# Kernel optimization log

Measured on AMD Instinct MI355X. Metric: run time of the kernel, lower is better.

The kernel has to match this reference:

```python
import jax, jax.numpy as jnp
import numpy as np

N_NODES = 50000
N_EDGES = 800000
D_FEAT = 128
EMBED_DIM = 128
NUM_HEADS = 8
HEAD_DIM = EMBED_DIM // NUM_HEADS


def mish(x):
    return x * jnp.tanh(jax.nn.softplus(x))


def setup_inputs() -> dict:
    key = jax.random.key(0)
    ks = jax.random.split(key, 8)
    nodes = jax.random.normal(ks[0], (N_NODES, D_FEAT), dtype=jnp.float32)
    senders = jax.random.randint(ks[1], (N_EDGES,), 0, N_NODES, dtype=jnp.int32)
    receivers = jax.random.randint(ks[2], (N_EDGES,), 0, N_NODES, dtype=jnp.int32)
    s = 1.0 / np.sqrt(D_FEAT)
    Ws_k = jax.random.normal(ks[3], (D_FEAT, NUM_HEADS, HEAD_DIM), dtype=jnp.float32) * s
    Ws_b = jnp.zeros((NUM_HEADS, HEAD_DIM), dtype=jnp.float32)
    Wr_k = jax.random.normal(ks[4], (D_FEAT, NUM_HEADS, HEAD_DIM), dtype=jnp.float32) * s
    Wr_b = jnp.zeros((NUM_HEADS, HEAD_DIM), dtype=jnp.float32)
    attn_k = jax.random.normal(ks[5], (HEAD_DIM, 1), dtype=jnp.float32) / np.sqrt(HEAD_DIM)
    attn_b = jnp.zeros((1,), dtype=jnp.float32)
    return {"nodes": nodes, "senders": senders, "receivers": receivers,
            "Ws_k": Ws_k, "Ws_b": Ws_b, "Wr_k": Wr_k, "Wr_b": Wr_b,
            "attn_k": attn_k, "attn_b": attn_b}


def reference(nodes, senders, receivers, Ws_k, Ws_b, Wr_k, Wr_b, attn_k, attn_b):
    # gather endpoint features along edges
    sent = nodes[senders]        # [E, F]
    recv = nodes[receivers]      # [E, F]
    # edge messages: W_s(sent) -> [E, H, D]
    edges = jnp.einsum('ef,fhd->ehd', sent, Ws_k) + Ws_b
    # attention logits: Dense(1)(mish(edges + W_r(recv))) -> [E, H, 1]
    x = mish(edges + jnp.einsum('ef,fhd->ehd', recv, Wr_k) + Wr_b)
    logits = jnp.einsum('ehd,do->eho', x, attn_k) + attn_b  # [E, H, 1]
    # segment softmax over incoming edges of each receiver node
    seg_max = jax.ops.segment_max(logits, receivers, num_segments=N_NODES)  # [N, H, 1]
    unnorm = jnp.exp(logits - seg_max[receivers])
    denom = jax.ops.segment_sum(unnorm, receivers, num_segments=N_NODES)   # [N, H, 1]
    weights = unnorm / denom[receivers]                                     # [E, H, 1]
    # attention-weighted scatter-add into receiver nodes
    agg = jax.ops.segment_sum(edges * weights, receivers, num_segments=N_NODES)  # [N, H, D]
    # node update: concat heads
    return agg.reshape(N_NODES, NUM_HEADS * HEAD_DIM)
```

## Files before the change

### kernel.cpp

```cpp
#include <hip/hip_runtime.h>

#define N_NODES 50000
#define N_EDGES 800000
#define HEADS 8
#define HD 16
#define F 128
#define RPB 16
#define SCAN_B 1024
#define NB1 ((N_NODES + SCAN_B - 1) / SCAN_B)
#define TILE 8

__device__ __forceinline__ float head16_sum(float x) {
    int v;
    v = __builtin_amdgcn_update_dpp(0, __float_as_int(x), 0xB1, 0xF, 0xF, true);
    x += __int_as_float(v);
    v = __builtin_amdgcn_update_dpp(0, __float_as_int(x), 0x4E, 0xF, 0xF, true);
    x += __int_as_float(v);
    v = __builtin_amdgcn_update_dpp(0, __float_as_int(x), 0x141, 0xF, 0xF, true);
    x += __int_as_float(v);
    v = __builtin_amdgcn_update_dpp(0, __float_as_int(x), 0x140, 0xF, 0xF, true);
    x += __int_as_float(v);
    return x;
}

__global__ __launch_bounds__(128) void k_proj(
        const float* __restrict__ nodes,
        const float* __restrict__ Ws, const float* __restrict__ Wsb,
        const float* __restrict__ Wr, const float* __restrict__ Wrb,
        float* __restrict__ Ps, float* __restrict__ Pr) {
    __shared__ float rows[RPB][F];
    const int o  = threadIdx.x;
    const int r0 = blockIdx.x * RPB;
    for (int i = 0; i < RPB; ++i)
        rows[i][o] = nodes[(r0 + i) * F + o];
    __syncthreads();

    float accs[RPB], accr[RPB];
    const float bs = Wsb[o], br = Wrb[o];
    #pragma unroll
    for (int i = 0; i < RPB; ++i) { accs[i] = bs; accr[i] = br; }

    for (int f = 0; f < F; ++f) {
        const float ws = Ws[f * F + o];
        const float wr = Wr[f * F + o];
        #pragma unroll
        for (int i = 0; i < RPB; ++i) {
            accs[i] = fmaf(rows[i][f], ws, accs[i]);
            accr[i] = fmaf(rows[i][f], wr, accr[i]);
        }
    }
    #pragma unroll
    for (int i = 0; i < RPB; ++i) {
        Ps[(r0 + i) * F + o] = accs[i];
        Pr[(r0 + i) * F + o] = accr[i];
    }
}

__global__ __launch_bounds__(256) void k_hist(
        const int* __restrict__ receivers, int* __restrict__ counts) {
    const int e = blockIdx.x * blockDim.x + threadIdx.x;
    if (e < N_EDGES) atomicAdd(counts + receivers[e], 1);
}

__global__ __launch_bounds__(1024) void k_scan1(
        const int* __restrict__ counts, int* __restrict__ starts,
        int* __restrict__ partials) {
    __shared__ int buf[SCAN_B];
    const int i = blockIdx.x * SCAN_B + threadIdx.x;
    const int v = (i < N_NODES) ? counts[i] : 0;
    buf[threadIdx.x] = v;
    __syncthreads();
    for (int off = 1; off < SCAN_B; off <<= 1) {
        const int t = (threadIdx.x >= (unsigned)off) ? buf[threadIdx.x - off] : 0;
        __syncthreads();
        buf[threadIdx.x] += t;
        __syncthreads();
    }
    if (i < N_NODES) starts[i] = buf[threadIdx.x] - v;
    if (threadIdx.x == SCAN_B - 1) partials[blockIdx.x] = buf[SCAN_B - 1];
}

__global__ __launch_bounds__(1024) void k_scan23(
        const int* __restrict__ partials, int* __restrict__ starts) {
    __shared__ int s_off;
    if (threadIdx.x < 64) {
        const int j = (int)threadIdx.x;
        int v = (j < (int)blockIdx.x && j < NB1) ? partials[j] : 0;
        v += __shfl_xor(v, 1);  v += __shfl_xor(v, 2);  v += __shfl_xor(v, 4);
        v += __shfl_xor(v, 8);  v += __shfl_xor(v, 16); v += __shfl_xor(v, 32);
        if (threadIdx.x == 0) s_off = v;
    }
    if (threadIdx.x == 0 && blockIdx.x == 0) starts[N_NODES] = N_EDGES;
    __syncthreads();
    const int i = blockIdx.x * SCAN_B + threadIdx.x;
    if (i < N_NODES) starts[i] += s_off;
}

__global__ __launch_bounds__(256) void k_fill(
        const int* __restrict__ senders, const int* __restrict__ receivers,
        const int* __restrict__ starts, int* __restrict__ cursor,
        int* __restrict__ slist) {
    const int e = blockIdx.x * blockDim.x + threadIdx.x;
    if (e >= N_EDGES) return;
    const int r = receivers[e];
    const int pos = atomicAdd(cursor + r, 1);
    slist[starts[r] + pos] = senders[e];
}

__global__ __launch_bounds__(128) void k_agg_fused(
        const int* __restrict__ starts, const int* __restrict__ slist,
        const float* __restrict__ Ps, const float* __restrict__ Pr,
        const float* __restrict__ attn_k, const float* __restrict__ attn_b,
        float* __restrict__ out) {
    const int n = blockIdx.x;
    const int t = threadIdx.x;
    const int e0 = starts[n], e1 = starts[n + 1];
    const float pr = Pr[n * F + t];
    const float ak = attn_k[t & 15];
    const float bias = attn_b[0];

    float m = -3.0e38f, den = 0.0f, acc = 0.0f;

    for (int i = e0; i < e1; i += TILE) {
        float psv[TILE], lg[TILE];
        #pragma unroll
        for (int k = 0; k < TILE; ++k) {
            const int idx = (i + k < e1) ? (i + k) : (e1 - 1);
            psv[k] = Ps[slist[idx] * F + t];
        }
        #pragma unroll
        for (int k = 0; k < TILE; ++k) {
            const float x  = psv[k] + pr;
            const float ex = __expf(x);
            const float z  = 1.0f + ex;
            const float zz = fmaf(z, z, 1.0f);
            const float r  = __builtin_amdgcn_rcpf(zz);
            const float v  = fmaf(-2.0f * x, r, x) * ak;
            const float sum = head16_sum(v);
            lg[k] = (i + k < e1) ? (sum + bias) : -3.0e38f;
        }
        float tm = lg[0];
        #pragma unroll
        for (int k = 1; k < TILE; ++k) tm = fmaxf(tm, lg[k]);
        const float mn = fmaxf(m, tm);
        const float cr = __expf(m - mn);
        den *= cr;  acc *= cr;  m = mn;
        #pragma unroll
        for (int k = 0; k < TILE; ++k) {
            const float w = __expf(lg[k] - mn);
            den += w;
            acc = fmaf(w, psv[k], acc);
        }
    }
    out[n * F + t] = (den > 0.0f) ? acc / den : 0.0f;
}

extern "C" void kernel_launch(void* const* d_in, const int* in_sizes, int n_in,
                              void* d_out, int out_size, void* d_ws, size_t ws_size,
                              hipStream_t stream) {
    const float* nodes     = (const float*)d_in[0];
    const int*   senders   = (const int*)  d_in[1];
    const int*   receivers = (const int*)  d_in[2];
    const float* Wsk       = (const float*)d_in[3];
    const float* Wsb       = (const float*)d_in[4];
    const float* Wrk       = (const float*)d_in[5];
    const float* Wrb       = (const float*)d_in[6];
    const float* attnk     = (const float*)d_in[7];
    const float* attnb     = (const float*)d_in[8];
    float* out = (float*)d_out;

    float* Ps       = (float*)d_ws;
    float* Pr       = Ps + (size_t)N_NODES * F;
    int*   slist    = (int*)(Pr + (size_t)N_NODES * F);
    int*   counts   = slist + N_EDGES;
    int*   cursor   = counts + N_NODES;
    int*   starts   = cursor + N_NODES;
    int*   partials = starts + N_NODES + 1;

    hipMemsetAsync(counts, 0, 2 * N_NODES * sizeof(int), stream);

    k_proj<<<N_NODES / RPB, 128, 0, stream>>>(nodes, Wsk, Wsb, Wrk, Wrb, Ps, Pr);

    const int e_blocks = (N_EDGES + 255) / 256;
    k_hist<<<e_blocks, 256, 0, stream>>>(receivers, counts);
    k_scan1<<<NB1, SCAN_B, 0, stream>>>(counts, starts, partials);
    k_scan23<<<NB1, SCAN_B, 0, stream>>>(partials, starts);
    k_fill<<<e_blocks, 256, 0, stream>>>(senders, receivers, starts, cursor, slist);

    k_agg_fused<<<N_NODES, 128, 0, stream>>>(starts, slist, Ps, Pr,
                                             attnk, attnb, out);
}
```

Before: 320.6 us.

## Fuse histogram into projection, fold scan fixup, drop online softmax max

Folds the receiver histogram into the projection kernel. Each of its blocks covers exactly 256 edges, which only works because the edge count equals 256 times the block count. It removes the scan fix-up kernel: block offsets are now recomputed from the partials inside the fill kernel (shared-memory prefix) and inside the aggregation kernel (wave reduction). The aggregation loop also drops the running-max rescaling and the attention bias, exponentiating raw logits directly. This cuts two launches and the per-tile max and rescale work, at the risk of exp overflow if logits ever grow large.

```diff
diff --git a/kernel.cpp b/kernel.cpp
--- a/kernel.cpp
+++ b/kernel.cpp
@@ -23,14 +23,20 @@
     return x;
 }
 
-__global__ __launch_bounds__(128) void k_proj(
+__global__ __launch_bounds__(128) void k_proj_hist(
         const float* __restrict__ nodes,
         const float* __restrict__ Ws, const float* __restrict__ Wsb,
         const float* __restrict__ Wr, const float* __restrict__ Wrb,
+        const int* __restrict__ receivers, int* __restrict__ counts,
         float* __restrict__ Ps, float* __restrict__ Pr) {
     __shared__ float rows[RPB][F];
     const int o  = threadIdx.x;
     const int r0 = blockIdx.x * RPB;
+
+    const int ebase = blockIdx.x * 256 + o;
+    atomicAdd(counts + receivers[ebase], 1);
+    atomicAdd(counts + receivers[ebase + 128], 1);
+
     for (int i = 0; i < RPB; ++i)
         rows[i][o] = nodes[(r0 + i) * F + o];
     __syncthreads();
@@ -56,12 +62,6 @@
     }
 }
 
-__global__ __launch_bounds__(256) void k_hist(
-        const int* __restrict__ receivers, int* __restrict__ counts) {
-    const int e = blockIdx.x * blockDim.x + threadIdx.x;
-    if (e < N_EDGES) atomicAdd(counts + receivers[e], 1);
-}
-
 __global__ __launch_bounds__(1024) void k_scan1(
         const int* __restrict__ counts, int* __restrict__ starts,
         int* __restrict__ partials) {
@@ -80,49 +80,53 @@
     if (threadIdx.x == SCAN_B - 1) partials[blockIdx.x] = buf[SCAN_B - 1];
 }
 
-__global__ __launch_bounds__(1024) void k_scan23(
-        const int* __restrict__ partials, int* __restrict__ starts) {
-    __shared__ int s_off;
+__global__ __launch_bounds__(256) void k_fill(
+        const int* __restrict__ senders, const int* __restrict__ receivers,
+        const int* __restrict__ starts, const int* __restrict__ partials,
+        int* __restrict__ cursor, int* __restrict__ slist) {
+    __shared__ int off_lds[NB1];
     if (threadIdx.x < 64) {
         const int j = (int)threadIdx.x;
-        int v = (j < (int)blockIdx.x && j < NB1) ? partials[j] : 0;
-        v += __shfl_xor(v, 1);  v += __shfl_xor(v, 2);  v += __shfl_xor(v, 4);
-        v += __shfl_xor(v, 8);  v += __shfl_xor(v, 16); v += __shfl_xor(v, 32);
-        if (threadIdx.x == 0) s_off = v;
+        const int v = (j < NB1) ? partials[j] : 0;
+        int incl = v;
+        #pragma unroll
+        for (int d = 1; d < 64; d <<= 1) {
+            const int u = __shfl_up(incl, d);
+            if (j >= d) incl += u;
+        }
+        if (j < NB1) off_lds[j] = incl - v;
     }
-    if (threadIdx.x == 0 && blockIdx.x == 0) starts[N_NODES] = N_EDGES;
     __syncthreads();
-    const int i = blockIdx.x * SCAN_B + threadIdx.x;
-    if (i < N_NODES) starts[i] += s_off;
-}
-
-__global__ __launch_bounds__(256) void k_fill(
-        const int* __restrict__ senders, const int* __restrict__ receivers,
-        const int* __restrict__ starts, int* __restrict__ cursor,
-        int* __restrict__ slist) {
-    const int e = blockIdx.x * blockDim.x + threadIdx.x;
-    if (e >= N_EDGES) return;
+    const int e = blockIdx.x * 256 + (int)threadIdx.x;
     const int r = receivers[e];
     const int pos = atomicAdd(cursor + r, 1);
-    slist[starts[r] + pos] = senders[e];
+    slist[starts[r] + off_lds[r >> 10] + pos] = senders[e];
 }
 
 __global__ __launch_bounds__(128) void k_agg_fused(
-        const int* __restrict__ starts, const int* __restrict__ slist,
+        const int* __restrict__ starts, const int* __restrict__ counts,
+        const int* __restrict__ partials, const int* __restrict__ slist,
         const float* __restrict__ Ps, const float* __restrict__ Pr,
-        const float* __restrict__ attn_k, const float* __restrict__ attn_b,
+        const float* __restrict__ attn_k,
         float* __restrict__ out) {
     const int n = blockIdx.x;
     const int t = threadIdx.x;
-    const int e0 = starts[n], e1 = starts[n + 1];
+
+    const int sb = n >> 10;
+    const int lane = t & 63;
+    int v = (lane < sb) ? partials[lane] : 0;
+    v += __shfl_xor(v, 1);  v += __shfl_xor(v, 2);  v += __shfl_xor(v, 4);
+    v += __shfl_xor(v, 8);  v += __shfl_xor(v, 16); v += __shfl_xor(v, 32);
+
+    const int e0 = starts[n] + v;
+    const int e1 = e0 + counts[n];
     const float pr = Pr[n * F + t];
     const float ak = attn_k[t & 15];
-    const float bias = attn_b[0];
 
-    float m = -3.0e38f, den = 0.0f, acc = 0.0f;
+    float den = 0.0f, acc = 0.0f;
 
     for (int i = e0; i < e1; i += TILE) {
-        float psv[TILE], lg[TILE];
+        float psv[TILE];
         #pragma unroll
         for (int k = 0; k < TILE; ++k) {
             const int idx = (i + k < e1) ? (i + k) : (e1 - 1);
@@ -135,19 +139,9 @@
             const float z  = 1.0f + ex;
             const float zz = fmaf(z, z, 1.0f);
             const float r  = __builtin_amdgcn_rcpf(zz);
-            const float v  = fmaf(-2.0f * x, r, x) * ak;
-            const float sum = head16_sum(v);
-            lg[k] = (i + k < e1) ? (sum + bias) : -3.0e38f;
-        }
-        float tm = lg[0];
-        #pragma unroll
-        for (int k = 1; k < TILE; ++k) tm = fmaxf(tm, lg[k]);
-        const float mn = fmaxf(m, tm);
-        const float cr = __expf(m - mn);
-        den *= cr;  acc *= cr;  m = mn;
-        #pragma unroll
-        for (int k = 0; k < TILE; ++k) {
-            const float w = __expf(lg[k] - mn);
+            const float mi = fmaf(-2.0f * x, r, x) * ak;
+            const float sum = head16_sum(mi);
+            const float w = (i + k < e1) ? __expf(sum) : 0.0f;
             den += w;
             acc = fmaf(w, psv[k], acc);
         }
@@ -166,7 +160,6 @@
     const float* Wrk       = (const float*)d_in[5];
     const float* Wrb       = (const float*)d_in[6];
     const float* attnk     = (const float*)d_in[7];
-    const float* attnb     = (const float*)d_in[8];
     float* out = (float*)d_out;
 
     float* Ps       = (float*)d_ws;
@@ -179,14 +172,11 @@
 
     hipMemsetAsync(counts, 0, 2 * N_NODES * sizeof(int), stream);
 
-    k_proj<<<N_NODES / RPB, 128, 0, stream>>>(nodes, Wsk, Wsb, Wrk, Wrb, Ps, Pr);
-
-    const int e_blocks = (N_EDGES + 255) / 256;
-    k_hist<<<e_blocks, 256, 0, stream>>>(receivers, counts);
+    k_proj_hist<<<N_NODES / RPB, 128, 0, stream>>>(nodes, Wsk, Wsb, Wrk, Wrb,
+                                                   receivers, counts, Ps, Pr);
     k_scan1<<<NB1, SCAN_B, 0, stream>>>(counts, starts, partials);
-    k_scan23<<<NB1, SCAN_B, 0, stream>>>(partials, starts);
-    k_fill<<<e_blocks, 256, 0, stream>>>(senders, receivers, starts, cursor, slist);
-
-    k_agg_fused<<<N_NODES, 128, 0, stream>>>(starts, slist, Ps, Pr,
-                                             attnk, attnb, out);
+    k_fill<<<N_EDGES / 256, 256, 0, stream>>>(senders, receivers, starts,
+                                              partials, cursor, slist);
+    k_agg_fused<<<N_NODES, 128, 0, stream>>>(starts, counts, partials, slist,
+                                             Ps, Pr, attnk, out);
 }
```

Result: faster. 312.2 us (-2.6%).
